# Kernel optimization log

Hardware: AMD Instinct MI355X
Metric: run time of the kernel (lower is better)

The kernel has to match this reference:

```python
import jax, jax.numpy as jnp
import numpy as np
from jax import lax

D = 2048
B = 8
T = 1024

def setup_inputs() -> dict:
    key = jax.random.key(0)
    ks = jax.random.split(key, 6)
    s = 1.0 / np.sqrt(D)
    return {
        "x": jax.random.normal(ks[0], (B, T, D), dtype=jnp.float32),
        "h0": jnp.zeros((B, D), dtype=jnp.float32),
        "W_in": jax.random.normal(ks[1], (D, D), dtype=jnp.float32) * s,
        "W_x": jax.random.normal(ks[2], (D, D), dtype=jnp.float32) * s,
        "W_h": jax.random.normal(ks[3], (D, D), dtype=jnp.float32) * (0.5 * s),
        "b": jnp.zeros((D,), dtype=jnp.float32),
        "log_alpha": jnp.asarray(np.log(0.5), dtype=jnp.float32),
        "W_out": jax.random.normal(ks[4], (D, D), dtype=jnp.float32) * s,
    }


def reference(x, h0, W_in, W_x, W_h, b, log_alpha, W_out):
    # x: [B,T,D] -> in_proj + silu pre-activation
    u = jax.nn.silu(jnp.einsum('btd,ed->bte', x, W_in))  # [B,T,D]
    alpha = jnp.exp(log_alpha)
    # Precompute input contribution for all steps: [T,B,D]
    wx_all = jnp.einsum('btd,ed->tbe', u, W_x) + b

    def step(h_prev, wx_t):
        pre = h_prev @ W_h.T + wx_t                  # [B,D]
        h_new = h_prev + alpha * jnp.tanh(pre)
        out = h_new * jax.nn.silu(h_new)             # self-gating
        return h_new, out

    _, outs = lax.scan(step, h0, wx_all)             # outs: [T,B,D]
    y = jnp.einsum('tbd,ed->bte', outs, W_out)       # out_proj -> [B,T,D]
    return y
```

## Files before the change

kernel.cpp:

```cpp
#include <hip/hip_runtime.h>

#define DEV static __device__ __forceinline__

typedef _Float16 half8  __attribute__((ext_vector_type(8)));
typedef _Float16 half4v __attribute__((ext_vector_type(4)));
typedef float    floatx4 __attribute__((ext_vector_type(4)));
typedef unsigned int u32;
typedef unsigned long long u64;
typedef u32 u32x4 __attribute__((ext_vector_type(4)));

#define SPLIT_S 1024.0f
#define SPLIT_R (1.0f / 1024.0f)

DEV void gl_lds16(const _Float16* g, _Float16* l) {
  __builtin_amdgcn_global_load_lds(
      (const __attribute__((address_space(1))) u32*)g,
      (__attribute__((address_space(3))) u32*)l, 16, 0, 0);
}

DEV u32x4 llc_load16(u64 addr) {
  u32x4 r;
  asm volatile("global_load_dwordx4 %0, %1, off sc0 sc1"
               : "=v"(r) : "v"(addr));
  return r;
}
DEV void mall_swap8(u64 addr, u64 v) {
  asm volatile("global_atomic_swap_x2 %0, %1, off"
               :: "v"(addr), "v"(v) : "memory");
}
DEV void mall_swap4(u64 addr, int v) {
  asm volatile("global_atomic_swap %0, %1, off"
               :: "v"(addr), "v"(v) : "memory");
}

DEV float fast_tanh(float x) {
  const float e = __expf(2.0f * fabsf(x));
  return copysignf(1.0f - 2.0f / (1.0f + e), x);
}

__global__ __launch_bounds__(256) void k_split_xw(
    const float* __restrict__ x, const float* __restrict__ win,
    _Float16* __restrict__ xhi, _Float16* __restrict__ xlo,
    _Float16* __restrict__ whi, _Float16* __restrict__ wlo)
{
  const int NX4 = (8192 * 2048) / 4;
  const int NW4 = (2048 * 2048) / 4;
  for (int i = blockIdx.x * 256 + threadIdx.x; i < NX4 + NW4; i += gridDim.x * 256) {
    const float* src; _Float16* dh; _Float16* dl; int j = i;
    if (j < NX4) { src = x; dh = xhi; dl = xlo; }
    else         { j -= NX4; src = win; dh = whi; dl = wlo; }
    const float4 v = ((const float4*)src)[j];
    half4v h, l;
#pragma unroll
    for (int q = 0; q < 4; ++q) {
      const float a = ((const float*)&v)[q];
      const _Float16 hh = (_Float16)a;
      h[q] = hh;
      l[q] = (_Float16)((a - (float)hh) * SPLIT_S);
    }
    ((half4v*)dh)[j] = h;
    ((half4v*)dl)[j] = l;
  }
}

__global__ __launch_bounds__(256) void k_convertB(
    const float* __restrict__ wx, const float* __restrict__ h0,
    _Float16* __restrict__ Wxhi, _Float16* __restrict__ Wxlo,
    char* __restrict__ hpub, int* __restrict__ flags)
{
  if (blockIdx.x == 0 && threadIdx.x < 128) flags[threadIdx.x] = 0;
  const int NW4 = (2048 * 2048) / 4;
  for (int i = blockIdx.x * 256 + threadIdx.x; i < NW4; i += gridDim.x * 256) {
    const float4 v = ((const float4*)wx)[i];
    half4v h, l;
#pragma unroll
    for (int j = 0; j < 4; ++j) {
      const float a = ((const float*)&v)[j];
      const _Float16 hh = (_Float16)a;
      h[j] = hh;
      l[j] = (_Float16)((a - (float)hh) * SPLIT_S);
    }
    ((half4v*)Wxhi)[i] = h;
    ((half4v*)Wxlo)[i] = l;
  }
  for (int id = blockIdx.x * 256 + threadIdx.x; id < 2048; id += gridDim.x * 256) {
    const int c = id >> 3, b = id & 7;
    union { _Float16 h[8]; u32x4 v; } hi, lo;
#pragma unroll
    for (int j = 0; j < 8; ++j) {
      const float v = h0[b * 2048 + c * 8 + j];
      const _Float16 h = (_Float16)v;
      hi.h[j] = h;
      lo.h[j] = (_Float16)((v - (float)h) * SPLIT_S);
    }
    *(u32x4*)(hpub + c * 128 + b * 16)         = hi.v;
    *(u32x4*)(hpub + 32768 + c * 128 + b * 16) = lo.v;
  }
}

__global__ __launch_bounds__(256) void k_convert2(
    const float* __restrict__ wout, _Float16* __restrict__ WoutF)
{
  const int NW4 = (2048 * 2048) / 4;
  for (int i = blockIdx.x * 256 + threadIdx.x; i < NW4; i += gridDim.x * 256) {
    const float4 v = ((const float4*)wout)[i];
    half4v o;
    o[0] = (_Float16)v.x; o[1] = (_Float16)v.y;
    o[2] = (_Float16)v.z; o[3] = (_Float16)v.w;
    ((half4v*)WoutF)[i] = o;
  }
}

template <int EPI>
__global__ __launch_bounds__(256) void k_gemm_ps(
    const _Float16* __restrict__ Ahi, const _Float16* __restrict__ Alo,
    const _Float16* __restrict__ Bhi, const _Float16* __restrict__ Blo,
    _Float16* __restrict__ Chi, _Float16* __restrict__ Clo,
    float* __restrict__ Cf, const float* __restrict__ bias,
    int M, int N, int K)
{
  __shared__ _Float16 Ah[4096], Al[4096], Bh[4096], Bl[4096];
  const int tid  = threadIdx.x;
  const int lane = tid & 63, wave = tid >> 6;
  const int wm = wave >> 1, wn = wave & 1;
  const int tm = blockIdx.y * 128, tn = blockIdx.x * 128;
  const int lr = lane & 15, lk = lane >> 4;
  const int r0 = tid >> 2;
  const int c0 = (tid & 3) * 8;

  floatx4 acch[4][4] = {};
  floatx4 accl[4][4] = {};

  for (int k0 = 0; k0 < K; k0 += 32) {
#pragma unroll
    for (int c = 0; c < 2; ++c) {
      const int row = c * 64 + r0;
      const size_t aoff = (size_t)(tm + row) * K + k0 + c0;
      const size_t boff = (size_t)(tn + row) * K + k0 + c0;
      gl_lds16(Ahi + aoff, Ah + c * 2048 + wave * 512);
      gl_lds16(Alo + aoff, Al + c * 2048 + wave * 512);
      gl_lds16(Bhi + boff, Bh + c * 2048 + wave * 512);
      gl_lds16(Blo + boff, Bl + c * 2048 + wave * 512);
    }
    __syncthreads();

    half8 fah[4], fal[4], fbh[4], fbl[4];
#pragma unroll
    for (int mi = 0; mi < 4; ++mi) {
      const int off = (wm * 64 + mi * 16 + lr) * 32 + lk * 8;
      fah[mi] = *(const half8*)(Ah + off);
      fal[mi] = *(const half8*)(Al + off);
    }
#pragma unroll
    for (int ni = 0; ni < 4; ++ni) {
      const int off = (wn * 64 + ni * 16 + lr) * 32 + lk * 8;
      fbh[ni] = *(const half8*)(Bh + off);
      fbl[ni] = *(const half8*)(Bl + off);
    }
#pragma unroll
    for (int mi = 0; mi < 4; ++mi)
#pragma unroll
      for (int ni = 0; ni < 4; ++ni) {
        acch[mi][ni] = __builtin_amdgcn_mfma_f32_16x16x32_f16(fah[mi], fbh[ni], acch[mi][ni], 0, 0, 0);
        accl[mi][ni] = __builtin_amdgcn_mfma_f32_16x16x32_f16(
            fah[mi], fbl[ni],
            __builtin_amdgcn_mfma_f32_16x16x32_f16(fal[mi], fbh[ni], accl[mi][ni], 0, 0, 0),
            0, 0, 0);
      }
    __syncthreads();
  }

#pragma unroll
  for (int mi = 0; mi < 4; ++mi)
#pragma unroll
    for (int ni = 0; ni < 4; ++ni) {
      const int gcol = tn + wn * 64 + ni * 16 + lr;
#pragma unroll
      for (int r = 0; r < 4; ++r) {
        const int grow = tm + wm * 64 + mi * 16 + lk * 4 + r;
        const float v = acch[mi][ni][r] + accl[mi][ni][r] * SPLIT_R;
        if (EPI == 0) {
          const float s = v / (1.0f + __expf(-v));
          const _Float16 sh = (_Float16)s;
          Chi[(size_t)grow * N + gcol] = sh;
          Clo[(size_t)grow * N + gcol] = (_Float16)((s - (float)sh) * SPLIT_S);
        } else {
          const int tt = grow & 1023, bb = grow >> 10;
          Cf[(size_t)(tt * 8 + bb) * N + gcol] = v + bias[gcol];
        }
      }
    }
}

__global__ __launch_bounds__(256) void k_gemm_out(
    const _Float16* __restrict__ A, const _Float16* __restrict__ B,
    float* __restrict__ C, int M, int N, int K)
{
  __shared__ _Float16 As[4096];
  __shared__ _Float16 Bs[4096];
  const int tid  = threadIdx.x;
  const int lane = tid & 63, wave = tid >> 6;
  const int wm = wave >> 1, wn = wave & 1;
  const int tm = blockIdx.y * 128, tn = blockIdx.x * 128;
  const int lr = lane & 15, lk = lane >> 4;
  const int r0 = tid >> 2;
  const int c0 = (tid & 3) * 8;

  floatx4 acc[4][4] = {};

  for (int k0 = 0; k0 < K; k0 += 32) {
#pragma unroll
    for (int c = 0; c < 2; ++c) {
      const int row = c * 64 + r0;
      gl_lds16(A + (size_t)(tm + row) * K + k0 + c0, As + c * 2048 + wave * 512);
      gl_lds16(B + (size_t)(tn + row) * K + k0 + c0, Bs + c * 2048 + wave * 512);
    }
    __syncthreads();

    half8 af[4], bf[4];
#pragma unroll
    for (int mi = 0; mi < 4; ++mi)
      af[mi] = *(const half8*)(As + (wm * 64 + mi * 16 + lr) * 32 + lk * 8);
#pragma unroll
    for (int ni = 0; ni < 4; ++ni)
      bf[ni] = *(const half8*)(Bs + (wn * 64 + ni * 16 + lr) * 32 + lk * 8);
#pragma unroll
    for (int mi = 0; mi < 4; ++mi)
#pragma unroll
      for (int ni = 0; ni < 4; ++ni)
        acc[mi][ni] = __builtin_amdgcn_mfma_f32_16x16x32_f16(af[mi], bf[ni], acc[mi][ni], 0, 0, 0);
    __syncthreads();
  }

#pragma unroll
  for (int mi = 0; mi < 4; ++mi)
#pragma unroll
    for (int ni = 0; ni < 4; ++ni) {
      const int gcol = tn + wn * 64 + ni * 16 + lr;
#pragma unroll
      for (int r = 0; r < 4; ++r) {
        const int grow = tm + wm * 64 + mi * 16 + lk * 4 + r;
        C[(size_t)grow * N + gcol] = acc[mi][ni][r] * 8.0f;
      }
    }
}

__global__ __launch_bounds__(256, 1) void k_recur(
    const float* __restrict__ Wh, const float* __restrict__ wxp,
    const float* __restrict__ h0p, const float* __restrict__ lalpha,
    _Float16* __restrict__ outs, char* __restrict__ h_pub, int* flags)
{
  __shared__ float red[256 * 4];
  const int tid = threadIdx.x;
  const int lane = tid & 63, wave = tid >> 6;
  const int g = blockIdx.x;
  const int e0 = g * 16;
  const int lr = lane & 15, lk = lane >> 4;
  const int lrc = lr & 7;
  const float alpha = __expf(lalpha[0]);

  half8 afh[16], afl[16];
#pragma unroll
  for (int ks = 0; ks < 16; ++ks) {
    const float* wp = Wh + (size_t)(e0 + lr) * 2048 + wave * 512 + ks * 32 + lk * 8;
    const float4 f0 = *(const float4*)wp;
    const float4 f1 = *(const float4*)(wp + 4);
    half8 h, l;
#pragma unroll
    for (int j = 0; j < 4; ++j) {
      const float a0 = ((const float*)&f0)[j], a1 = ((const float*)&f1)[j];
      const _Float16 h0_ = (_Float16)a0;
      const _Float16 h1_ = (_Float16)a1;
      h[j]     = h0_; l[j]     = (_Float16)((a0 - (float)h0_) * SPLIT_S);
      h[j + 4] = h1_; l[j + 4] = (_Float16)((a1 - (float)h1_) * SPLIT_S);
    }
    afh[ks] = h; afl[ks] = l;
  }

  const bool owner = (tid < 64) && (lr < 8);
  float hr0 = 0.f, hr1 = 0.f, hr2 = 0.f, hr3 = 0.f;
  if (owner) {
    const float4 hv = *(const float4*)(h0p + (size_t)lr * 2048 + e0 + lk * 4);
    hr0 = hv.x; hr1 = hv.y; hr2 = hv.z; hr3 = hv.w;
  }

  const u64 hbase = (u64)h_pub;
  const u64 flag_base = (u64)flags;
  const u64 gb_off = (u64)((wave * 64 + lk) * 128 + lrc * 16);

  for (int t = 0; t < 1024; ++t) {
    float4 wv = {0.f, 0.f, 0.f, 0.f};
    if (owner) wv = *(const float4*)(wxp + (size_t)(t * 8 + lr) * 2048 + e0 + lk * 4);

    if (t > 0 && wave == 0) {
      const u64* fp = (const u64*)flags + lane;
      for (;;) {
        const u64 fv = __hip_atomic_load(fp, __ATOMIC_RELAXED, __HIP_MEMORY_SCOPE_AGENT);
        if (__all(((int)fv >= t) && ((int)(fv >> 32) >= t))) break;
        __builtin_amdgcn_s_sleep(1);
      }
    }
    __syncthreads();

    const u64 pb = hbase + (u64)(t & 1) * 65536 + gb_off;
    u32x4 sh[16], sl[16];
#pragma unroll
    for (int ks = 0; ks < 16; ++ks) sh[ks] = llc_load16(pb + (u64)ks * 512);
#pragma unroll
    for (int ks = 0; ks < 16; ++ks) sl[ks] = llc_load16(pb + 32768 + (u64)ks * 512);
    asm volatile("s_waitcnt vmcnt(16)" ::: "memory");
    __builtin_amdgcn_sched_barrier(0);

    floatx4 ph[4] = {};
    floatx4 pl[4] = {};
#pragma unroll
    for (int ks = 0; ks < 16; ++ks) {
      const half8 bh = __builtin_bit_cast(half8, sh[ks]);
      ph[ks & 3] = __builtin_amdgcn_mfma_f32_16x16x32_f16(afh[ks], bh, ph[ks & 3], 0, 0, 0);
      pl[ks & 3] = __builtin_amdgcn_mfma_f32_16x16x32_f16(afl[ks], bh, pl[ks & 3], 0, 0, 0);
    }
    asm volatile("s_waitcnt vmcnt(0)" ::: "memory");
    __builtin_amdgcn_sched_barrier(0);

#pragma unroll
    for (int ks = 0; ks < 16; ++ks) {
      const half8 bl = __builtin_bit_cast(half8, sl[ks]);
      pl[ks & 3] = __builtin_amdgcn_mfma_f32_16x16x32_f16(afh[ks], bl, pl[ks & 3], 0, 0, 0);
    }
    const floatx4 pt = (ph[0] + ph[1] + ph[2] + ph[3]) +
                       (pl[0] + pl[1] + pl[2] + pl[3]) * SPLIT_R;
    *(floatx4*)&red[(wave * 64 + lane) * 4] = pt;
    __syncthreads();

    if (tid < 64) {
      const floatx4* R = (const floatx4*)red;
      const floatx4 s = R[lane] + R[64 + lane] + R[128 + lane] + R[192 + lane];
      union { _Float16 h[4]; u64 u; } hv, lv, ov;
      if (owner) {
        hr0 += alpha * fast_tanh(s[0] + wv.x);
        hr1 += alpha * fast_tanh(s[1] + wv.y);
        hr2 += alpha * fast_tanh(s[2] + wv.z);
        hr3 += alpha * fast_tanh(s[3] + wv.w);
        hv.h[0] = (_Float16)hr0; hv.h[1] = (_Float16)hr1;
        hv.h[2] = (_Float16)hr2; hv.h[3] = (_Float16)hr3;
        lv.h[0] = (_Float16)((hr0 - (float)hv.h[0]) * SPLIT_S);
        lv.h[1] = (_Float16)((hr1 - (float)hv.h[1]) * SPLIT_S);
        lv.h[2] = (_Float16)((hr2 - (float)hv.h[2]) * SPLIT_S);
        lv.h[3] = (_Float16)((hr3 - (float)hv.h[3]) * SPLIT_S);
        const u64 dst = hbase + (u64)((t + 1) & 1) * 65536 +
                        (u64)((2 * g + (lk >> 1)) * 128 + lr * 16 + (lk & 1) * 8);
        mall_swap8(dst,         hv.u);
        mall_swap8(dst + 32768, lv.u);
      }
      asm volatile("s_waitcnt vmcnt(0)" ::: "memory");
      if (lane == 0) mall_swap4(flag_base + (u64)g * 4, t + 1);
      if (owner) {
        ov.h[0] = (_Float16)((hr0 * hr0 / (1.f + __expf(-hr0))) * 0.125f);
        ov.h[1] = (_Float16)((hr1 * hr1 / (1.f + __expf(-hr1))) * 0.125f);
        ov.h[2] = (_Float16)((hr2 * hr2 / (1.f + __expf(-hr2))) * 0.125f);
        ov.h[3] = (_Float16)((hr3 * hr3 / (1.f + __expf(-hr3))) * 0.125f);
        *(u64*)(outs + (size_t)(lr * 1024 + t) * 2048 + e0 + lk * 4) = ov.u;
      }
    }
  }
}

extern "C" void kernel_launch(void* const* d_in, const int* in_sizes, int n_in,
                              void* d_out, int out_size, void* d_ws, size_t ws_size,
                              hipStream_t stream)
{
  (void)in_sizes; (void)n_in; (void)out_size; (void)ws_size;
  const float* x    = (const float*)d_in[0];
  const float* h0   = (const float*)d_in[1];
  const float* Win  = (const float*)d_in[2];
  const float* Wx   = (const float*)d_in[3];
  const float* Wh   = (const float*)d_in[4];
  const float* bias = (const float*)d_in[5];
  const float* lal  = (const float*)d_in[6];
  const float* Wout = (const float*)d_in[7];

  char* ws = (char*)d_ws;
  _Float16* Uhi   = (_Float16*)(ws);
  _Float16* Ulo   = (_Float16*)(ws + 33554432);
  _Float16* OUTS  = (_Float16*)(ws);
  _Float16* WoutF = (_Float16*)(ws + 33554432);
  _Float16* Whi   = (_Float16*)(ws + 67108864);
  _Float16* Wlo   = (_Float16*)(ws + 75497472);
  char*     hpub  = ws + 83886080;
  int*      flags = (int*)(ws + 84017152);
  _Float16* xhi   = (_Float16*)d_out;
  _Float16* xlo   = (_Float16*)((char*)d_out + 33554432);
  float*    wxbuf = (float*)d_out;

  const dim3 gg(16, 64);

  k_split_xw<<<2048, 256, 0, stream>>>(x, Win, xhi, xlo, Whi, Wlo);
  k_gemm_ps<0><<<gg, 256, 0, stream>>>(xhi, xlo, Whi, Wlo, Uhi, Ulo,
                                       nullptr, nullptr, 8192, 2048, 2048);
  k_convertB<<<512, 256, 0, stream>>>(Wx, h0, Whi, Wlo, hpub, flags);
  k_gemm_ps<1><<<gg, 256, 0, stream>>>(Uhi, Ulo, Whi, Wlo, nullptr, nullptr,
                                       wxbuf, bias, 8192, 2048, 2048);
  k_convert2<<<512, 256, 0, stream>>>(Wout, WoutF);
  k_recur<<<128, 256, 0, stream>>>(Wh, wxbuf, h0, lal, OUTS, hpub, flags);
  k_gemm_out<<<gg, 256, 0, stream>>>(OUTS, WoutF, (float*)d_out, 8192, 2048, 2048);
}
```

Before: 4.179 ms.

## Spread recurrence epilogue across all waves and pipeline flag polling loads

The per-step tanh update, fp16 hi/lo split and publish of h move from a single wave to lanes 0-7 of each of the four waves, so the serial epilogue on the critical path is shorter. A block barrier is added before one thread publishes the step flag. Flag polling now keeps two outstanding LLC-coherent loads in flight instead of one atomic load followed by a sleep, which is meant to cut the latency of noticing other blocks' progress. The cost is an extra __syncthreads per step and more global polling traffic.

```diff
diff --git a/kernel.cpp b/kernel.cpp
--- a/kernel.cpp
+++ b/kernel.cpp
@@ -277,10 +277,10 @@
     afh[ks] = h; afl[ks] = l;
   }
 
-  const bool owner = (tid < 64) && (lr < 8);
+  const bool owner = (lane < 8);
   float hr0 = 0.f, hr1 = 0.f, hr2 = 0.f, hr3 = 0.f;
   if (owner) {
-    const float4 hv = *(const float4*)(h0p + (size_t)lr * 2048 + e0 + lk * 4);
+    const float4 hv = *(const float4*)(h0p + (size_t)lane * 2048 + e0 + wave * 4);
     hr0 = hv.x; hr1 = hv.y; hr2 = hv.z; hr3 = hv.w;
   }
 
@@ -290,15 +290,26 @@
 
   for (int t = 0; t < 1024; ++t) {
     float4 wv = {0.f, 0.f, 0.f, 0.f};
-    if (owner) wv = *(const float4*)(wxp + (size_t)(t * 8 + lr) * 2048 + e0 + lk * 4);
+    if (owner) wv = *(const float4*)(wxp + (size_t)(t * 8 + lane) * 2048 + e0 + wave * 4);
 
     if (t > 0 && wave == 0) {
-      const u64* fp = (const u64*)flags + lane;
+      const u64 fp = flag_base + (u64)lane * 8;
+      u64 f1, f2;
+      asm volatile("global_load_dwordx2 %0, %1, off sc0 sc1" : "=v"(f1) : "v"(fp));
+      __builtin_amdgcn_s_sleep(4);
+      asm volatile("global_load_dwordx2 %0, %1, off sc0 sc1" : "=v"(f2) : "v"(fp));
       for (;;) {
-        const u64 fv = __hip_atomic_load(fp, __ATOMIC_RELAXED, __HIP_MEMORY_SCOPE_AGENT);
-        if (__all(((int)fv >= t) && ((int)(fv >> 32) >= t))) break;
-        __builtin_amdgcn_s_sleep(1);
+        asm volatile("s_waitcnt vmcnt(1)" ::: "memory");
+        __builtin_amdgcn_sched_barrier(0);
+        if (__all(((int)f1 >= t) && ((int)(f1 >> 32) >= t))) break;
+        asm volatile("global_load_dwordx2 %0, %1, off sc0 sc1" : "=v"(f1) : "v"(fp));
+        asm volatile("s_waitcnt vmcnt(1)" ::: "memory");
+        __builtin_amdgcn_sched_barrier(0);
+        if (__all(((int)f2 >= t) && ((int)(f2 >> 32) >= t))) break;
+        asm volatile("global_load_dwordx2 %0, %1, off sc0 sc1" : "=v"(f2) : "v"(fp));
       }
+      asm volatile("s_waitcnt vmcnt(0)" ::: "memory");
+      __builtin_amdgcn_sched_barrier(0);
     }
     __syncthreads();
 
@@ -332,36 +343,35 @@
     *(floatx4*)&red[(wave * 64 + lane) * 4] = pt;
     __syncthreads();
 
-    if (tid < 64) {
+    union { _Float16 h[4]; u64 u; } hv, lv, ov;
+    if (owner) {
       const floatx4* R = (const floatx4*)red;
-      const floatx4 s = R[lane] + R[64 + lane] + R[128 + lane] + R[192 + lane];
-      union { _Float16 h[4]; u64 u; } hv, lv, ov;
-      if (owner) {
-        hr0 += alpha * fast_tanh(s[0] + wv.x);
-        hr1 += alpha * fast_tanh(s[1] + wv.y);
-        hr2 += alpha * fast_tanh(s[2] + wv.z);
-        hr3 += alpha * fast_tanh(s[3] + wv.w);
-        hv.h[0] = (_Float16)hr0; hv.h[1] = (_Float16)hr1;
-        hv.h[2] = (_Float16)hr2; hv.h[3] = (_Float16)hr3;
-        lv.h[0] = (_Float16)((hr0 - (float)hv.h[0]) * SPLIT_S);
-        lv.h[1] = (_Float16)((hr1 - (float)hv.h[1]) * SPLIT_S);
-        lv.h[2] = (_Float16)((hr2 - (float)hv.h[2]) * SPLIT_S);
-        lv.h[3] = (_Float16)((hr3 - (float)hv.h[3]) * SPLIT_S);
-        const u64 dst = hbase + (u64)((t + 1) & 1) * 65536 +
-                        (u64)((2 * g + (lk >> 1)) * 128 + lr * 16 + (lk & 1) * 8);
-        mall_swap8(dst,         hv.u);
-        mall_swap8(dst + 32768, lv.u);
-      }
-      asm volatile("s_waitcnt vmcnt(0)" ::: "memory");
-      if (lane == 0) mall_swap4(flag_base + (u64)g * 4, t + 1);
-      if (owner) {
-        ov.h[0] = (_Float16)((hr0 * hr0 / (1.f + __expf(-hr0))) * 0.125f);
-        ov.h[1] = (_Float16)((hr1 * hr1 / (1.f + __expf(-hr1))) * 0.125f);
-        ov.h[2] = (_Float16)((hr2 * hr2 / (1.f + __expf(-hr2))) * 0.125f);
-        ov.h[3] = (_Float16)((hr3 * hr3 / (1.f + __expf(-hr3))) * 0.125f);
-        *(u64*)(outs + (size_t)(lr * 1024 + t) * 2048 + e0 + lk * 4) = ov.u;
-      }
-    }
+      const int fi = wave * 16 + lane;
+      const floatx4 s = R[fi] + R[64 + fi] + R[128 + fi] + R[192 + fi];
+      hr0 += alpha * fast_tanh(s[0] + wv.x);
+      hr1 += alpha * fast_tanh(s[1] + wv.y);
+      hr2 += alpha * fast_tanh(s[2] + wv.z);
+      hr3 += alpha * fast_tanh(s[3] + wv.w);
+      hv.h[0] = (_Float16)hr0; hv.h[1] = (_Float16)hr1;
+      hv.h[2] = (_Float16)hr2; hv.h[3] = (_Float16)hr3;
+      lv.h[0] = (_Float16)((hr0 - (float)hv.h[0]) * SPLIT_S);
+      lv.h[1] = (_Float16)((hr1 - (float)hv.h[1]) * SPLIT_S);
+      lv.h[2] = (_Float16)((hr2 - (float)hv.h[2]) * SPLIT_S);
+      lv.h[3] = (_Float16)((hr3 - (float)hv.h[3]) * SPLIT_S);
+      const u64 dst = hbase + (u64)((t + 1) & 1) * 65536 +
+                      (u64)((2 * g + (wave >> 1)) * 128 + lane * 16 + (wave & 1) * 8);
+      mall_swap8(dst,         hv.u);
+      mall_swap8(dst + 32768, lv.u);
+      ov.h[0] = (_Float16)((hr0 * hr0 / (1.f + __expf(-hr0))) * 0.125f);
+      ov.h[1] = (_Float16)((hr1 * hr1 / (1.f + __expf(-hr1))) * 0.125f);
+      ov.h[2] = (_Float16)((hr2 * hr2 / (1.f + __expf(-hr2))) * 0.125f);
+      ov.h[3] = (_Float16)((hr3 * hr3 / (1.f + __expf(-hr3))) * 0.125f);
+    }
+    asm volatile("s_waitcnt vmcnt(0)" ::: "memory");
+    __syncthreads();
+    if (tid == 0) mall_swap4(flag_base + (u64)g * 4, t + 1);
+    if (owner)
+      *(u64*)(outs + (size_t)(lane * 1024 + t) * 2048 + e0 + wave * 4) = ov.u;
   }
 }
 
```

Result: slower. 7.087 ms (+69.6%).
